# Performance work log

Measured on AMD Instinct MI355X. Metric: run time of the kernel, lower is better.

Reference implementation:

```python
import jax, jax.numpy as jnp
import numpy as np

VIEW_R = 32
SCALING = 16.0 / 8.0  # lora_alpha / r


def setup_inputs() -> dict:
    key = jax.random.key(0)
    ks = jax.random.split(key, 12)
    bs, S, d, r = 64, 256, 768, 8
    n = d // VIEW_R  # 24
    return {
        "x": jax.random.normal(ks[0], (bs, S, d), jnp.float32),
        "user_h": jax.random.normal(ks[1], (bs, d), jnp.float32),
        "item_h": jax.random.normal(ks[2], (bs, d), jnp.float32),
        "W": jax.random.normal(ks[3], (d, d), jnp.float32) * 0.02,   # base weight (out,in)
        "b": jax.random.normal(ks[4], (d,), jnp.float32) * 0.02,
        "A": jax.random.normal(ks[5], (r, d), jnp.float32) * 0.02,   # lora_A
        "B": jax.random.normal(ks[6], (d, r), jnp.float32) * 0.02,   # lora_B (zeros at init; randomized to exercise math)
        "Wu": jax.random.normal(ks[7], (d, d), jnp.float32) * 0.02,  # lora_U weight (out,in)
        "VU": jax.random.normal(ks[8], (n, VIEW_R), jnp.float32) * 0.02,
        "Wi": jax.random.normal(ks[9], (d, d), jnp.float32) * 0.02,  # lora_I weight
        "VI": jax.random.normal(ks[10], (n, VIEW_R), jnp.float32) * 0.02,
    }


def _kron_branch(x, h, Wlin, V):
    # original: weight[b, q*n_in + n, l*32 + m] = (h @ Wlin.T)[b, q, l] * V[n, m]
    #           result[b,s,:] = x[b,s,:] @ weight[b]
    # factorized form (same math, no (bs, d, d) intermediate):
    bs, S, d = x.shape
    n, m = V.shape
    q = VIEW_R
    l = d // VIEW_R
    wq = (h @ Wlin.T).reshape(bs, q, l)          # (b, q, l)
    x4 = x.reshape(bs, S, q, n)                  # d split as (q, n)
    t = jnp.einsum("bsqn,nm->bsqm", x4, V)
    out = jnp.einsum("bsqm,bql->bslm", t, wq)    # out index = l*32 + m
    return out.reshape(bs, S, d)


def reference(x, user_h, item_h, W, b, A, B, Wu, VU, Wi, VI):
    # F.linear + LoRA
    out = jnp.einsum("bsd,od->bso", x, W) + b
    out = out + jnp.einsum("bsd,rd,or->bso", x, A, B) * SCALING
    # user Kronecker low-rank per-sample weight branch
    out = out + _kron_branch(x, user_h, Wu, VU)
    # item branch
    out = out + _kron_branch(x, item_h, Wi, VI)
    return out
```

## Files before the change

kernel.cpp:

```cpp
#include <hip/hip_runtime.h>
#include <hip/hip_bf16.h>

typedef __bf16 bf16x8 __attribute__((ext_vector_type(8)));
typedef float f32x4 __attribute__((ext_vector_type(4)));
typedef unsigned short u16x8 __attribute__((ext_vector_type(8)));

__device__ __forceinline__ unsigned short f2bf(float f) {
    unsigned int u = __builtin_bit_cast(unsigned int, f);
    unsigned int r = (u + 0x7FFFu + ((u >> 16) & 1u)) >> 16;
    return (unsigned short)r;
}

__device__ __forceinline__ void load_lds_16(const void* g, void* lds) {
    __builtin_amdgcn_global_load_lds(
        (const __attribute__((address_space(1))) unsigned int*)g,
        (__attribute__((address_space(3))) unsigned int*)lds, 16, 0, 0);
}

__global__ __launch_bounds__(256) void prep_kernel(
    const float* __restrict__ x, unsigned short* __restrict__ xb,
    const float* __restrict__ W, const float* __restrict__ A,
    const float* __restrict__ B, unsigned short* __restrict__ weffB,
    const float* __restrict__ uh, const float* __restrict__ ih,
    const float* __restrict__ Wu, const float* __restrict__ Wi,
    float* __restrict__ wqu_p, float* __restrict__ wqi_p) {
    __shared__ __align__(16) float Wl[64 * 100];
    __shared__ __align__(16) float Hl[32 * 100];
    const int bx = blockIdx.x;
    const int t = threadIdx.x;
    if (bx < 384) {
        const int g = bx % 24, j = bx / 24;
        const int br = g / 12, ot = g % 12;
        const int bt = j & 1, ks = j >> 1;
        const int o0 = ot * 64, b0 = bt * 32, k0 = ks * 96;
        const float* h = (br ? ih : uh);
        const float* Wm = (br ? Wi : Wu);
        for (int i = t; i < 1536; i += 256) {
            int row = i / 24, c = i % 24;
            *(float4*)&Wl[row * 100 + c * 4] =
                *(const float4*)(Wm + (size_t)(o0 + row) * 768 + k0 + c * 4);
        }
        for (int i = t; i < 768; i += 256) {
            int row = i / 24, c = i % 24;
            *(float4*)&Hl[row * 100 + c * 4] =
                *(const float4*)(h + (size_t)(b0 + row) * 768 + k0 + c * 4);
        }
        __syncthreads();
        const int o2 = t & 31, b4 = t >> 5;
        float acc[2][4] = {};
#pragma unroll 6
        for (int k4 = 0; k4 < 24; ++k4) {
            float4 w0 = *(const float4*)&Wl[o2 * 100 + k4 * 4];
            float4 w1 = *(const float4*)&Wl[(o2 + 32) * 100 + k4 * 4];
#pragma unroll
            for (int jj = 0; jj < 4; ++jj) {
                float4 hb = *(const float4*)&Hl[(b4 * 4 + jj) * 100 + k4 * 4];
                acc[0][jj] += w0.x * hb.x + w0.y * hb.y + w0.z * hb.z + w0.w * hb.w;
                acc[1][jj] += w1.x * hb.x + w1.y * hb.y + w1.z * hb.z + w1.w * hb.w;
            }
        }
        float* part = (br ? wqi_p : wqu_p) + (size_t)ks * 49152;
#pragma unroll
        for (int oo = 0; oo < 2; ++oo)
#pragma unroll
            for (int jj = 0; jj < 4; ++jj)
                part[(size_t)(b0 + b4 * 4 + jj) * 768 + o0 + o2 + oo * 32] = acc[oo][jj];
    } else if (bx < 2688) {
        int idx = bx - 384;
        int o = idx / 3;
        int k = (idx % 3) * 256 + t;
        float acc = W[o * 768 + k];
#pragma unroll
        for (int r = 0; r < 8; ++r) acc += 2.0f * B[o * 8 + r] * A[r * 768 + k];
        weffB[o * 768 + k] = f2bf(acc);
    } else {
        int b2 = bx - 2688;
        const float4* xp = (const float4*)x;
        float4 a[4], c[4];
        int i0 = b2 * 1024 + t;
#pragma unroll
        for (int u = 0; u < 4; ++u) {
            int i = i0 + u * 256;
            a[u] = xp[i * 2];
            c[u] = xp[i * 2 + 1];
        }
#pragma unroll
        for (int u = 0; u < 4; ++u) {
            int i = i0 + u * 256;
            u16x8 r;
            r[0] = f2bf(a[u].x); r[1] = f2bf(a[u].y); r[2] = f2bf(a[u].z); r[3] = f2bf(a[u].w);
            r[4] = f2bf(c[u].x); r[5] = f2bf(c[u].y); r[6] = f2bf(c[u].z); r[7] = f2bf(c[u].w);
            *(u16x8*)(xb + (size_t)i * 8) = r;
        }
    }
}

__global__ __launch_bounds__(256, 3) void gemm_fused_kernel(
    const unsigned short* __restrict__ Xb, const unsigned short* __restrict__ WeffB,
    const float* __restrict__ VU, const float* __restrict__ VI,
    const float* __restrict__ wqu_p, const float* __restrict__ wqi_p,
    const float* __restrict__ bias, float* __restrict__ out) {
    __shared__ __align__(16) unsigned short As[128 * 64];
    __shared__ __align__(16) unsigned short Bs[128 * 64];
    __shared__ __align__(16) unsigned int vui[32 * 26];
    __shared__ __align__(16) float wqs[32 * 8];
    __shared__ float bias_s[128];
    const int tid = threadIdx.x;
    const int wave = tid >> 6, lane = tid & 63;
    const int id = blockIdx.x;
    const int nt = id >> 7, rem = id & 127, b = rem >> 1, mt = rem & 1;
    const int s0 = mt * 128, n0 = nt * 128;

    for (int i = tid; i < 768; i += 256) {
        int n = i >> 5, m = i & 31;
        vui[m * 26 + n] = ((unsigned int)f2bf(VU[i]) << 16) | (unsigned int)f2bf(VI[i]);
    }
    {
        int q = tid >> 3, g = (tid >> 1) & 3, brs = tid & 1;
        const float* p = (brs ? wqi_p : wqu_p) + b * 768 + q * 24 + nt * 4 + g;
        float s = 0.0f;
#pragma unroll
        for (int ks = 0; ks < 8; ++ks) s += p[(size_t)ks * 49152];
        wqs[tid] = s;
    }
    if (tid < 128) bias_s[tid] = bias[n0 + tid];
    __syncthreads();

    const unsigned short* Abase = Xb + (size_t)(b * 256 + s0) * 768;
    const unsigned short* Bbase = WeffB + (size_t)n0 * 768;
    const int wm = wave & 1, wn = wave >> 1;
    const int lrow = lane >> 3, lcp = lane & 7;
    const int rg = tid >> 3, cc = tid & 7;
    const int sl = cc ^ (rg & 7);
    const unsigned short* Wp0 = Bbase + (size_t)rg * 768 + cc * 8;

    f32x4 acc[4][4] = {};
    u16x8 wreg[4];
#pragma unroll
    for (int g = 0; g < 4; ++g) wreg[g] = *(const u16x8*)(Wp0 + (size_t)g * 32 * 768);

    for (int kk = 0; kk < 768; kk += 64) {
#pragma unroll
        for (int u = 0; u < 4; ++u) {
            int tA = wave * 4 + u;
            int r = tA * 8 + lrow;
            int c = lcp ^ (r & 7);
            load_lds_16(Abase + (size_t)r * 768 + kk + c * 8, (void*)(As + tA * 512));
        }
        {
            int kb = kk + cc * 8;
            int q = (kb * 2731) >> 16;
            int n0c = kb - q * 24;
            const unsigned int* vp = &vui[rg * 26 + n0c];
            uint2 pv01 = *(const uint2*)(vp);
            uint2 pv23 = *(const uint2*)(vp + 2);
            uint2 pv45 = *(const uint2*)(vp + 4);
            uint2 pv67 = *(const uint2*)(vp + 6);
            unsigned int pv[8] = {pv01.x, pv01.y, pv23.x, pv23.y, pv45.x, pv45.y, pv67.x, pv67.y};
            float fu[8], fi[8];
#pragma unroll
            for (int j = 0; j < 8; ++j) {
                fu[j] = __builtin_bit_cast(float, pv[j] & 0xFFFF0000u);
                fi[j] = __builtin_bit_cast(float, pv[j] << 16);
            }
            const float4* wp4 = (const float4*)&wqs[q * 8];
            float4 wa = wp4[0], wb = wp4[1];
            float wu[4] = {wa.x, wa.z, wb.x, wb.z};
            float wi[4] = {wa.y, wa.w, wb.y, wb.w};
#pragma unroll
            for (int g = 0; g < 4; ++g) {
                uint4 wd = __builtin_bit_cast(uint4, wreg[g]);
                unsigned int warr[4] = {wd.x, wd.y, wd.z, wd.w};
                unsigned int kvw[4];
#pragma unroll
                for (int p = 0; p < 4; ++p) {
                    float lo = __builtin_bit_cast(float, warr[p] << 16);
                    float hi = __builtin_bit_cast(float, warr[p] & 0xFFFF0000u);
                    float v0 = fmaf(fi[2 * p],     wi[g], fmaf(fu[2 * p],     wu[g], lo));
                    float v1 = fmaf(fi[2 * p + 1], wi[g], fmaf(fu[2 * p + 1], wu[g], hi));
                    kvw[p] = __builtin_amdgcn_perm(__builtin_bit_cast(unsigned int, v1),
                                                   __builtin_bit_cast(unsigned int, v0),
                                                   0x07060302u);
                }
                *(uint4*)(Bs + (g * 32 + rg) * 64 + sl * 8) =
                    make_uint4(kvw[0], kvw[1], kvw[2], kvw[3]);
            }
        }
        if (kk < 704) {
            const unsigned short* Wn = Wp0 + kk + 64;
#pragma unroll
            for (int g = 0; g < 4; ++g) wreg[g] = *(const u16x8*)(Wn + (size_t)g * 32 * 768);
        }
        __syncthreads();
#pragma unroll
        for (int h = 0; h < 2; ++h) {
            const int cb = h * 4 + (lane >> 4);
            const int rl = lane & 15;
            bf16x8 af[4], bw[4];
#pragma unroll
            for (int i = 0; i < 4; ++i) {
                int r = wm * 64 + i * 16 + rl;
                int c = cb ^ (r & 7);
                af[i] = *(const bf16x8*)(As + r * 64 + c * 8);
            }
#pragma unroll
            for (int j = 0; j < 4; ++j) {
                int r = wn * 64 + j * 16 + rl;
                int c = cb ^ (r & 7);
                bw[j] = *(const bf16x8*)(Bs + r * 64 + c * 8);
            }
#pragma unroll
            for (int i = 0; i < 4; ++i)
#pragma unroll
                for (int j = 0; j < 4; ++j)
                    acc[i][j] = __builtin_amdgcn_mfma_f32_16x16x32_bf16(af[i], bw[j], acc[i][j], 0, 0, 0);
        }
        __syncthreads();
    }

    const int cl = lane & 15, rq = lane >> 4;
#pragma unroll
    for (int j = 0; j < 4; ++j) {
        int nn = wn * 64 + j * 16 + cl;
        float bv = bias_s[nn];
#pragma unroll
        for (int i = 0; i < 4; ++i) {
            int mrow = s0 + wm * 64 + i * 16 + rq * 4;
            float* op = out + (size_t)(b * 256 + mrow) * 768 + n0 + nn;
#pragma unroll
            for (int g = 0; g < 4; ++g) op[(size_t)g * 768] = acc[i][j][g] + bv;
        }
    }
}

__global__ void weff_kernel(const float* __restrict__ W, const float* __restrict__ A,
                            const float* __restrict__ B, float* __restrict__ Weff) {
    int o = blockIdx.x / 3;
    int k = (blockIdx.x % 3) * 256 + threadIdx.x;
    float acc = W[o * 768 + k];
#pragma unroll
    for (int r = 0; r < 8; ++r) acc += 2.0f * B[o * 8 + r] * A[r * 768 + k];
    Weff[o * 768 + k] = acc;
}

__global__ void wq2_kernel(const float* __restrict__ uh, const float* __restrict__ ih,
                           const float* __restrict__ Wu, const float* __restrict__ Wi,
                           float* __restrict__ wqu, float* __restrict__ wqi) {
    int bx = blockIdx.x;
    int og = bx % 192;
    int rest = bx / 192;
    int b = rest & 63;
    int br = rest >> 6;
    int wave = threadIdx.x >> 6, lane = threadIdx.x & 63;
    int o = og * 4 + wave;
    const float* h = (br ? ih : uh) + b * 768;
    const float* Wrow = (br ? Wi : Wu) + (size_t)o * 768;
    const float4* hp = (const float4*)(h + lane * 12);
    const float4* wp = (const float4*)(Wrow + lane * 12);
    float s = 0.0f;
#pragma unroll
    for (int j = 0; j < 3; ++j) {
        float4 hv = hp[j], wv = wp[j];
        s += hv.x * wv.x + hv.y * wv.y + hv.z * wv.z + hv.w * wv.w;
    }
#pragma unroll
    for (int off = 32; off; off >>= 1) s += __shfl_down(s, off);
    if (lane == 0) (br ? wqi : wqu)[b * 768 + o] = s;
}

__global__ void naive_kernel(const float* __restrict__ x, const float* __restrict__ Weff,
                             const float* __restrict__ wqu, const float* __restrict__ wqi,
                             const float* __restrict__ VU, const float* __restrict__ VI,
                             const float* __restrict__ bias, float* __restrict__ out) {
    int bs_ = blockIdx.x / 3;
    int chunk = blockIdx.x % 3;
    int b = bs_ >> 8;
    __shared__ float xs[768];
    for (int i = threadIdx.x; i < 768; i += 256) xs[i] = x[(size_t)bs_ * 768 + i];
    __syncthreads();
    int o = chunk * 256 + threadIdx.x;
    int m = o & 31, l = o >> 5;
    float acc = bias[o];
    for (int q = 0; q < 32; ++q) {
        float wu = wqu[b * 768 + q * 24 + l];
        float wi = wqi[b * 768 + q * 24 + l];
#pragma unroll
        for (int n = 0; n < 24; ++n) {
            int k = q * 24 + n;
            float w = Weff[o * 768 + k] + VU[n * 32 + m] * wu + VI[n * 32 + m] * wi;
            acc += xs[k] * w;
        }
    }
    out[(size_t)bs_ * 768 + o] = acc;
}

extern "C" void kernel_launch(void* const* d_in, const int* in_sizes, int n_in,
                              void* d_out, int out_size, void* d_ws, size_t ws_size,
                              hipStream_t stream) {
    const float* x  = (const float*)d_in[0];
    const float* uh = (const float*)d_in[1];
    const float* ih = (const float*)d_in[2];
    const float* W  = (const float*)d_in[3];
    const float* bv = (const float*)d_in[4];
    const float* A  = (const float*)d_in[5];
    const float* B  = (const float*)d_in[6];
    const float* Wu = (const float*)d_in[7];
    const float* VU = (const float*)d_in[8];
    const float* Wi = (const float*)d_in[9];
    const float* VI = (const float*)d_in[10];
    float* out = (float*)d_out;

    const size_t off_xb   = 0;
    const size_t off_weff = 25165824;
    const size_t off_wqu  = off_weff + 1179648;
    const size_t off_wqi  = off_wqu + 1572864;
    const size_t need     = off_wqi + 1572864;

    char* ws = (char*)d_ws;
    if (ws_size >= need) {
        unsigned short* xb    = (unsigned short*)(ws + off_xb);
        unsigned short* weffB = (unsigned short*)(ws + off_weff);
        float* wqu_p = (float*)(ws + off_wqu);
        float* wqi_p = (float*)(ws + off_wqi);
        prep_kernel<<<4224, 256, 0, stream>>>(x, xb, W, A, B, weffB, uh, ih, Wu, Wi, wqu_p, wqi_p);
        gemm_fused_kernel<<<768, 256, 0, stream>>>(xb, weffB, VU, VI, wqu_p, wqi_p, bv, out);
    } else {
        float* weff = (float*)ws;
        float* wqu  = weff + 589824;
        float* wqi  = wqu + 49152;
        weff_kernel<<<2304, 256, 0, stream>>>(W, A, B, weff);
        wq2_kernel<<<24576, 256, 0, stream>>>(uh, ih, Wu, Wi, wqu, wqi);
        naive_kernel<<<49152, 256, 0, stream>>>(x, weff, wqu, wqi, VU, VI, bv, out);
    }
}
```

Before: 150.3 us.

## Double-buffer the B tile and overlap next-tile build with MFMA compute

The B tile in LDS becomes double-buffered. The loop is restructured so the A fragments for the current step are read into registers first, then the async A load and the W register prefetch for the next step are issued, and the next B tile is built after the MFMAs. This is meant to hide global latency and the per-tile construction of the effective weights behind matrix work. In exchange it uses an extra 16KB of LDS and holds the A fragments live in registers, which may reduce occupancy below the 3-block launch bound.

```diff
diff --git a/kernel.cpp b/kernel.cpp
--- a/kernel.cpp
+++ b/kernel.cpp
@@ -101,7 +101,7 @@
     const float* __restrict__ wqu_p, const float* __restrict__ wqi_p,
     const float* __restrict__ bias, float* __restrict__ out) {
     __shared__ __align__(16) unsigned short As[128 * 64];
-    __shared__ __align__(16) unsigned short Bs[128 * 64];
+    __shared__ __align__(16) unsigned short Bs[2][128 * 64];
     __shared__ __align__(16) unsigned int vui[32 * 26];
     __shared__ __align__(16) float wqs[32 * 8];
     __shared__ float bias_s[128];
@@ -134,12 +134,49 @@
     const int sl = cc ^ (rg & 7);
     const unsigned short* Wp0 = Bbase + (size_t)rg * 768 + cc * 8;
 
-    f32x4 acc[4][4] = {};
     u16x8 wreg[4];
-#pragma unroll
-    for (int g = 0; g < 4; ++g) wreg[g] = *(const u16x8*)(Wp0 + (size_t)g * 32 * 768);
-
-    for (int kk = 0; kk < 768; kk += 64) {
+
+    auto build = [&](int kkb, unsigned short* bs_w) {
+        int kb = kkb + cc * 8;
+        int q = (kb * 2731) >> 16;
+        int n0c = kb - q * 24;
+        const unsigned int* vp = &vui[rg * 26 + n0c];
+        uint2 pv01 = *(const uint2*)(vp);
+        uint2 pv23 = *(const uint2*)(vp + 2);
+        uint2 pv45 = *(const uint2*)(vp + 4);
+        uint2 pv67 = *(const uint2*)(vp + 6);
+        unsigned int pv[8] = {pv01.x, pv01.y, pv23.x, pv23.y, pv45.x, pv45.y, pv67.x, pv67.y};
+        float fu[8], fi[8];
+#pragma unroll
+        for (int j = 0; j < 8; ++j) {
+            fu[j] = __builtin_bit_cast(float, pv[j] & 0xFFFF0000u);
+            fi[j] = __builtin_bit_cast(float, pv[j] << 16);
+        }
+        const float4* wp4 = (const float4*)&wqs[q * 8];
+        float4 wa = wp4[0], wb = wp4[1];
+        float wu[4] = {wa.x, wa.z, wb.x, wb.z};
+        float wi[4] = {wa.y, wa.w, wb.y, wb.w};
+#pragma unroll
+        for (int g = 0; g < 4; ++g) {
+            uint4 wd = __builtin_bit_cast(uint4, wreg[g]);
+            unsigned int warr[4] = {wd.x, wd.y, wd.z, wd.w};
+            unsigned int kvw[4];
+#pragma unroll
+            for (int p = 0; p < 4; ++p) {
+                float lo = __builtin_bit_cast(float, warr[p] << 16);
+                float hi = __builtin_bit_cast(float, warr[p] & 0xFFFF0000u);
+                float v0 = fmaf(fi[2 * p],     wi[g], fmaf(fu[2 * p],     wu[g], lo));
+                float v1 = fmaf(fi[2 * p + 1], wi[g], fmaf(fu[2 * p + 1], wu[g], hi));
+                kvw[p] = __builtin_amdgcn_perm(__builtin_bit_cast(unsigned int, v1),
+                                               __builtin_bit_cast(unsigned int, v0),
+                                               0x07060302u);
+            }
+            *(uint4*)(bs_w + (g * 32 + rg) * 64 + sl * 8) =
+                make_uint4(kvw[0], kvw[1], kvw[2], kvw[3]);
+        }
+    };
+
+    auto dma_A = [&](int kk) {
 #pragma unroll
         for (int u = 0; u < 4; ++u) {
             int tA = wave * 4 + u;
@@ -147,75 +184,56 @@
             int c = lcp ^ (r & 7);
             load_lds_16(Abase + (size_t)r * 768 + kk + c * 8, (void*)(As + tA * 512));
         }
-        {
-            int kb = kk + cc * 8;
-            int q = (kb * 2731) >> 16;
-            int n0c = kb - q * 24;
-            const unsigned int* vp = &vui[rg * 26 + n0c];
-            uint2 pv01 = *(const uint2*)(vp);
-            uint2 pv23 = *(const uint2*)(vp + 2);
-            uint2 pv45 = *(const uint2*)(vp + 4);
-            uint2 pv67 = *(const uint2*)(vp + 6);
-            unsigned int pv[8] = {pv01.x, pv01.y, pv23.x, pv23.y, pv45.x, pv45.y, pv67.x, pv67.y};
-            float fu[8], fi[8];
-#pragma unroll
-            for (int j = 0; j < 8; ++j) {
-                fu[j] = __builtin_bit_cast(float, pv[j] & 0xFFFF0000u);
-                fi[j] = __builtin_bit_cast(float, pv[j] << 16);
-            }
-            const float4* wp4 = (const float4*)&wqs[q * 8];
-            float4 wa = wp4[0], wb = wp4[1];
-            float wu[4] = {wa.x, wa.z, wb.x, wb.z};
-            float wi[4] = {wa.y, wa.w, wb.y, wb.w};
-#pragma unroll
-            for (int g = 0; g < 4; ++g) {
-                uint4 wd = __builtin_bit_cast(uint4, wreg[g]);
-                unsigned int warr[4] = {wd.x, wd.y, wd.z, wd.w};
-                unsigned int kvw[4];
-#pragma unroll
-                for (int p = 0; p < 4; ++p) {
-                    float lo = __builtin_bit_cast(float, warr[p] << 16);
-                    float hi = __builtin_bit_cast(float, warr[p] & 0xFFFF0000u);
-                    float v0 = fmaf(fi[2 * p],     wi[g], fmaf(fu[2 * p],     wu[g], lo));
-                    float v1 = fmaf(fi[2 * p + 1], wi[g], fmaf(fu[2 * p + 1], wu[g], hi));
-                    kvw[p] = __builtin_amdgcn_perm(__builtin_bit_cast(unsigned int, v1),
-                                                   __builtin_bit_cast(unsigned int, v0),
-                                                   0x07060302u);
-                }
-                *(uint4*)(Bs + (g * 32 + rg) * 64 + sl * 8) =
-                    make_uint4(kvw[0], kvw[1], kvw[2], kvw[3]);
-            }
-        }
-        if (kk < 704) {
-            const unsigned short* Wn = Wp0 + kk + 64;
-#pragma unroll
-            for (int g = 0; g < 4; ++g) wreg[g] = *(const u16x8*)(Wn + (size_t)g * 32 * 768);
-        }
+    };
+
+    dma_A(0);
+#pragma unroll
+    for (int g = 0; g < 4; ++g) wreg[g] = *(const u16x8*)(Wp0 + (size_t)g * 32 * 768);
+    build(0, &Bs[0][0]);
+
+    f32x4 acc[4][4] = {};
+
+    for (int t = 0; t < 12; ++t) {
+        const int kk = t * 64;
         __syncthreads();
+        bf16x8 af2[2][4];
 #pragma unroll
         for (int h = 0; h < 2; ++h) {
             const int cb = h * 4 + (lane >> 4);
             const int rl = lane & 15;
-            bf16x8 af[4], bw[4];
 #pragma unroll
             for (int i = 0; i < 4; ++i) {
                 int r = wm * 64 + i * 16 + rl;
                 int c = cb ^ (r & 7);
-                af[i] = *(const bf16x8*)(As + r * 64 + c * 8);
+                af2[h][i] = *(const bf16x8*)(As + r * 64 + c * 8);
             }
+        }
+        __syncthreads();
+        if (t < 11) {
+            dma_A(kk + 64);
+            const unsigned short* Wn = Wp0 + kk + 64;
+#pragma unroll
+            for (int g = 0; g < 4; ++g) wreg[g] = *(const u16x8*)(Wn + (size_t)g * 32 * 768);
+        }
+        const unsigned short* bs_r = &Bs[t & 1][0];
+#pragma unroll
+        for (int h = 0; h < 2; ++h) {
+            const int cb = h * 4 + (lane >> 4);
+            const int rl = lane & 15;
+            bf16x8 bw[4];
 #pragma unroll
             for (int j = 0; j < 4; ++j) {
                 int r = wn * 64 + j * 16 + rl;
                 int c = cb ^ (r & 7);
-                bw[j] = *(const bf16x8*)(Bs + r * 64 + c * 8);
+                bw[j] = *(const bf16x8*)(bs_r + r * 64 + c * 8);
             }
 #pragma unroll
             for (int i = 0; i < 4; ++i)
 #pragma unroll
                 for (int j = 0; j < 4; ++j)
-                    acc[i][j] = __builtin_amdgcn_mfma_f32_16x16x32_bf16(af[i], bw[j], acc[i][j], 0, 0, 0);
-        }
-        __syncthreads();
+                    acc[i][j] = __builtin_amdgcn_mfma_f32_16x16x32_bf16(af2[h][i], bw[j], acc[i][j], 0, 0, 0);
+        }
+        if (t < 11) build(kk + 64, &Bs[(t + 1) & 1][0]);
     }
 
     const int cl = lane & 15, rq = lane >> 4;
```

Measured after the change: 163.0 us. 8.4% more time.
